# Kernel optimization log

Measured on AMD Instinct MI355X. Metric: run time of the kernel, lower is better.

Reference implementation:

```python
import jax, jax.numpy as jnp
import numpy as np


def setup_inputs() -> dict:
    key = jax.random.key(0)
    B, DP, N = 4, 3, 8192
    positions = jax.random.normal(key, (B, DP, N), dtype=jnp.float32)
    return {"positions": positions, "k": 16}


def reference(positions, k):
    # positions: [B, Dp, N] ('simple' data_format)
    # Pairwise squared Euclidean distances between all N points per batch:
    # d2[b, i, j] = ||x_i - x_j||^2 = ||x_i||^2 + ||x_j||^2 - 2 x_i . x_j
    sq = jnp.sum(positions * positions, axis=1)                     # [B, N]
    dots = jnp.einsum('bdn,bdm->bnm', positions, positions)         # [B, N, N]
    d2 = sq[:, :, None] + sq[:, None, :] - 2.0 * dots               # [B, N, N]
    # k nearest neighbors (smallest distance; includes self at distance ~0)
    neg_d, idx = jax.lax.top_k(-d2, k)                              # [B, N, K]
    # Layer transposes raw op output [B, N, K] -> [B, K, N]
    NN = jnp.transpose(idx, (0, 2, 1)).astype(jnp.int32)            # [B, K, N]
    distances = jnp.transpose(-neg_d, (0, 2, 1))                    # [B, K, N]
    return (NN, distances)
```

## Files before the change

kernel.cpp:

```cpp
#include <hip/hip_runtime.h>
#include <stdint.h>

#define NPTS 8192
#define NPAIR 4096
#define NB 4
#define KNN 16
#define RQ 2
#define CCAP 20
#define DCAP 256
#define MARGIN 1.5e-3f

typedef unsigned long long u64;
typedef unsigned int u32;
typedef unsigned short u16;
typedef float f32x2 __attribute__((ext_vector_type(2)));

__device__ __forceinline__ u32 f2ord(float f) {
    u32 b = __float_as_uint(f);
    return (b & 0x80000000u) ? ~b : (b | 0x80000000u);
}
__device__ __forceinline__ float ord2f(u32 u) {
    u32 b = (u & 0x80000000u) ? (u & 0x7fffffffu) : ~u;
    return __uint_as_float(b);
}
__device__ __forceinline__ u64 shflx64(u64 v, int m) {
    u32 lo = (u32)v, hi = (u32)(v >> 32);
    lo = __shfl_xor(lo, m, 64);
    hi = __shfl_xor(hi, m, 64);
    return ((u64)hi << 32) | lo;
}

__global__ __launch_bounds__(256) void pack_kernel(const float* __restrict__ pos,
                                                   float4* __restrict__ pos8) {
    int t = blockIdx.x * 256 + threadIdx.x;
    int b = t >> 12;
    int m = t & (NPAIR - 1);
    const float* p = pos + (size_t)b * 3 * NPTS;
    float2 x = *(const float2*)&p[2 * m];
    float2 y = *(const float2*)&p[NPTS + 2 * m];
    float2 z = *(const float2*)&p[2 * NPTS + 2 * m];
    float s0 = __fadd_rn(__fadd_rn(__fmul_rn(x.x, x.x), __fmul_rn(y.x, y.x)), __fmul_rn(z.x, z.x));
    float s1 = __fadd_rn(__fadd_rn(__fmul_rn(x.y, x.y), __fmul_rn(y.y, y.y)), __fmul_rn(z.y, z.y));
    pos8[2 * t]     = make_float4(x.x, x.y, y.x, y.y);
    pos8[2 * t + 1] = make_float4(z.x, z.y, s0, s1);
}

#define RECOMP2(r, m, d0, d1)                                                           \
    { float4 _a = P8[2 * (m)], _c = P8[2 * (m) + 1];                                    \
      float _dot0 = __fmaf_rn(qzv[r].x, _c.x, __fmaf_rn(qyv[r].x, _a.z, __fmul_rn(qxv[r].x, _a.x))); \
      float _dot1 = __fmaf_rn(qzv[r].x, _c.y, __fmaf_rn(qyv[r].x, _a.w, __fmul_rn(qxv[r].x, _a.y))); \
      d0 = __fsub_rn(__fadd_rn(qw[r], _c.z), __fmul_rn(2.0f, _dot0));                   \
      d1 = __fsub_rn(__fadd_rn(qw[r], _c.w), __fmul_rn(2.0f, _dot1)); }

#define PROC(Av, Cv, mm)                                                                \
    {                                                                                   \
        f32x2 x01 = {(Av).x, (Av).y}, y01 = {(Av).z, (Av).w};                           \
        f32x2 z01 = {(Cv).x, (Cv).y}, sq01 = {(Cv).z, (Cv).w};                          \
        _Pragma("unroll")                                                               \
        for (int r = 0; r < RQ; ++r) {                                                  \
            f32x2 dot01 = __builtin_elementwise_fma(                                    \
                qzv[r], z01, __builtin_elementwise_fma(qyv[r], y01, qxv[r] * x01));     \
            f32x2 val01 = __builtin_elementwise_fma(n2v, dot01, sq01);                  \
            col[wv][r][c[r]][lane] = (u16)(mm);                                         \
            c[r] += (fminf(val01.x, val01.y) < Tm[r]) ? 1 : 0;                          \
        }                                                                               \
    }

__global__ __launch_bounds__(256) void knn_kernel(const float4* __restrict__ pos8,
                                                  float* __restrict__ out) {
    __shared__ u16 col[4][RQ][CCAP][64];
    __shared__ u16 dense[4][DCAP];
    const int lane = threadIdx.x & 63;
    const int wv = threadIdx.x >> 6;
    const int rowbase = blockIdx.x * (4 * RQ) + wv * RQ;
    const int b = rowbase >> 13;
    const int ib = rowbase & (NPTS - 1);
    const float4* __restrict__ P8 = pos8 + (size_t)b * NPAIR * 2;
    const u64 below = (1ull << lane) - 1ull;

    f32x2 qxv[RQ], qyv[RQ], qzv[RQ];
    float qw[RQ];
    {
        int m = ib >> 1;
        float4 a = P8[2 * m], cc = P8[2 * m + 1];
        qxv[0] = (f32x2){a.x, a.x};  qyv[0] = (f32x2){a.z, a.z};
        qzv[0] = (f32x2){cc.x, cc.x}; qw[0] = cc.z;
        qxv[1] = (f32x2){a.y, a.y};  qyv[1] = (f32x2){a.w, a.w};
        qzv[1] = (f32x2){cc.y, cc.y}; qw[1] = cc.w;
    }
    const f32x2 n2v = {-2.0f, -2.0f};

    float Tm[RQ];
    int c[RQ];

    auto rank16f = [&](float v) -> float {
#pragma unroll
        for (int k = 2; k <= 64; k <<= 1)
#pragma unroll
            for (int j = k >> 1; j >= 1; j >>= 1) {
                float o = __shfl_xor(v, j, 64);
                bool up = ((lane & k) == 0) == ((lane & j) == 0);
                v = (up ? (v < o) : (v > o)) ? v : o;
            }
        return __shfl(v, 15, 64);
    };

    auto tighten = [&](int r) {
        u32 mn = 0xFFFFFFFFu;
#pragma unroll
        for (int t = 0; t < CCAP; ++t) {
            if (t < c[r]) {
                u32 m = (u32)col[wv][r][t][lane];
                float d0, d1; RECOMP2(r, m, d0, d1);
                u32 om = f2ord(d0); u32 o1 = f2ord(d1);
                om = o1 < om ? o1 : om;
                mn = om < mn ? om : mn;
            }
        }
        u32 v = mn;
#pragma unroll
        for (int k = 2; k <= 64; k <<= 1)
#pragma unroll
            for (int j = k >> 1; j >= 1; j >>= 1) {
                u32 o = (u32)__shfl_xor((int)v, j, 64);
                bool up = ((lane & k) == 0) == ((lane & j) == 0);
                v = (up ? (v < o) : (v > o)) ? v : o;
            }
        u32 ordK = (u32)__shfl((int)v, 15, 64);
        int nc = 0;
#pragma unroll
        for (int t = 0; t < CCAP; ++t) {
            if (t < c[r]) {
                u32 m = (u32)col[wv][r][t][lane];
                float d0, d1; RECOMP2(r, m, d0, d1);
                u32 om = f2ord(d0); u32 o1 = f2ord(d1);
                om = o1 < om ? o1 : om;
                if (om <= ordK) { col[wv][r][nc][lane] = (u16)m; ++nc; }
            }
        }
        c[r] = nc;
#pragma unroll 1
        for (int it = 0; it < CCAP - 16; ++it) {
            if (c[r] > 16) {
                u64 mx = 0; int mt = 0;
#pragma unroll
                for (int t = 0; t < CCAP; ++t) {
                    if (t < c[r]) {
                        u32 m = (u32)col[wv][r][t][lane];
                        float d0, d1; RECOMP2(r, m, d0, d1);
                        u32 o0 = f2ord(d0), o1 = f2ord(d1);
                        u64 key = (o1 < o0)
                            ? (((u64)o1 << 13) | (2 * m + 1))
                            : (((u64)o0 << 13) | (2 * m));
                        if (key > mx) { mx = key; mt = t; }
                    }
                }
                col[wv][r][mt][lane] = col[wv][r][c[r] - 1][lane];
                c[r] -= 1;
            }
        }
        Tm[r] = fminf(Tm[r], (ord2f(ordK) - qw[r]) + MARGIN);
    };

    {
        float4 A[4], C[4];
#pragma unroll
        for (int s = 0; s < 4; ++s) {
            int m = s * 64 + lane;
            A[s] = P8[2 * m];
            C[s] = P8[2 * m + 1];
        }
#pragma unroll
        for (int r = 0; r < RQ; ++r) {
            f32x2 vv[4];
            float mn = __uint_as_float(0x7f800000u);
#pragma unroll
            for (int s = 0; s < 4; ++s) {
                f32x2 x01 = {A[s].x, A[s].y}, y01 = {A[s].z, A[s].w};
                f32x2 z01 = {C[s].x, C[s].y}, sq01 = {C[s].z, C[s].w};
                vv[s] = __builtin_elementwise_fma(
                    n2v, __builtin_elementwise_fma(qzv[r], z01,
                         __builtin_elementwise_fma(qyv[r], y01, qxv[r] * x01)), sq01);
                mn = fminf(mn, fminf(vv[s].x, vv[s].y));
            }
            float V16 = rank16f(mn);
            Tm[r] = V16 + 2.0f * MARGIN;
            c[r] = 0;
#pragma unroll
            for (int s = 0; s < 4; ++s) {
                int m = s * 64 + lane;
                col[wv][r][c[r]][lane] = (u16)m;
                c[r] += (fminf(vv[s].x, vv[s].y) < Tm[r]) ? 1 : 0;
            }
        }
    }

#pragma unroll 1
    for (int g = 1; g < 16; ++g) {
        if (__ballot(c[0] > 16)) tighten(0);
        if (__ballot(c[1] > 16)) tighten(1);
        int base = g * 256;
        float4 A[4], C[4];
#pragma unroll
        for (int s = 0; s < 4; ++s) {
            int m = base + s * 64 + lane;
            A[s] = P8[2 * m];
            C[s] = P8[2 * m + 1];
        }
        PROC(A[0], C[0], base + lane);
        PROC(A[1], C[1], base + 64 + lane);
        PROC(A[2], C[2], base + 128 + lane);
        PROC(A[3], C[3], base + 192 + lane);
    }

#pragma unroll
    for (int r = 0; r < RQ; ++r) {
        int sum = c[r];
#pragma unroll
        for (int s2 = 1; s2 < 64; s2 <<= 1) sum += __shfl_xor(sum, s2, 64);
        if (sum > 32) tighten(r);
        int nc = 0;
#pragma unroll 1
        for (int t = 0; t < CCAP; ++t) {
            bool valid = t < c[r];
            u64 bal = __ballot(valid);
            if (!bal) break;
            if (valid) dense[wv][nc + (int)__popcll(bal & below)] = col[wv][r][t][lane];
            nc += (int)__popcll(bal);
        }
        u64 myk = ~0ULL;
        if (nc <= 32) {
            bool valid = lane < 2 * nc;
            u32 m = valid ? (u32)dense[wv][lane >> 1] : 0u;
            float d0, d1; RECOMP2(r, m, d0, d1);
            float dd = (lane & 1) ? d1 : d0;
            u64 v = valid ? (((u64)f2ord(dd) << 13) | (2 * m + (lane & 1))) : ~0ULL;
#pragma unroll
            for (int k = 2; k <= 64; k <<= 1)
#pragma unroll
                for (int j = k >> 1; j >= 1; j >>= 1) {
                    u64 o = shflx64(v, j);
                    bool up = ((lane & k) == 0) == ((lane & j) == 0);
                    v = (up ? (v < o) : (v > o)) ? v : o;
                }
            myk = v;
        } else {
            u64 s8[8];
#pragma unroll
            for (int t = 0; t < 4; ++t) {
                int bi = t * 64 + lane;
                bool valid = bi < nc;
                u32 m = valid ? (u32)dense[wv][bi] : 0u;
                float d0, d1; RECOMP2(r, m, d0, d1);
                s8[2 * t]     = valid ? (((u64)f2ord(d0) << 13) | (2 * m))     : ~0ULL;
                s8[2 * t + 1] = valid ? (((u64)f2ord(d1) << 13) | (2 * m + 1)) : ~0ULL;
            }
#pragma unroll 1
            for (int rr = 0; rr < KNN; ++rr) {
                u64 lm = s8[0];
#pragma unroll
                for (int t = 1; t < 8; ++t) lm = s8[t] < lm ? s8[t] : lm;
                u64 mm = lm;
#pragma unroll
                for (int s2 = 1; s2 < 64; s2 <<= 1) { u64 o = shflx64(mm, s2); mm = o < mm ? o : mm; }
#pragma unroll
                for (int t = 0; t < 8; ++t) s8[t] = (s8[t] == mm) ? ~0ULL : s8[t];
                if (lane == rr) myk = mm;
            }
        }
        if (lane < KNN) {
            int iq = ib + r;
            size_t o1 = (size_t)(b * KNN + lane) * NPTS + iq;
            out[o1] = (float)(u32)(myk & (u64)(NPTS - 1));
            out[(size_t)NB * KNN * NPTS + o1] = ord2f((u32)(myk >> 13));
        }
    }
}

extern "C" void kernel_launch(void* const* d_in, const int* in_sizes, int n_in,
                              void* d_out, int out_size, void* d_ws, size_t ws_size,
                              hipStream_t stream) {
    const float* pos = (const float*)d_in[0];
    float* out = (float*)d_out;
    float4* pos8 = (float4*)d_ws;

    pack_kernel<<<dim3(NB * NPAIR / 256), dim3(256), 0, stream>>>(pos, pos8);
    knn_kernel<<<dim3(NB * NPTS / 8), dim3(256), 0, stream>>>(pos8, out);
}
```

Baseline: 164.0 us.

## Stage candidate point tiles in double-buffered shared memory with prefetch

Before, each wave loaded all 256 candidate points of a tile straight from global memory, so the four waves of a block fetched the same data four times. Now the block loads each tile once, one point per thread, into SoA shared-memory buffers. The next tile is prefetched into registers while the current one is processed, and a block-wide barrier runs after every tile. This cuts redundant global/L2 traffic and hides load latency, at the cost of 8KB of LDS, per-tile __syncthreads, and waves becoming coupled even though tighten() is called per wave.

Result: no change. 166.3 us (+1.4%).

```diff
diff --git a/kernel.cpp b/kernel.cpp
--- a/kernel.cpp
+++ b/kernel.cpp
@@ -52,26 +52,29 @@
       d0 = __fsub_rn(__fadd_rn(qw[r], _c.z), __fmul_rn(2.0f, _dot0));                   \
       d1 = __fsub_rn(__fadd_rn(qw[r], _c.w), __fmul_rn(2.0f, _dot1)); }
 
-#define PROC(Av, Cv, mm)                                                                \
+#define PROCL(cur, s, gbase)                                                            \
     {                                                                                   \
-        f32x2 x01 = {(Av).x, (Av).y}, y01 = {(Av).z, (Av).w};                           \
-        f32x2 z01 = {(Cv).x, (Cv).y}, sq01 = {(Cv).z, (Cv).w};                          \
+        int idx = (s) * 64 + lane;                                                      \
+        f32x2 x01 = sxA[cur][idx], y01 = syA[cur][idx];                                 \
+        f32x2 z01 = szA[cur][idx], sq01 = sqA[cur][idx];                                \
         _Pragma("unroll")                                                               \
         for (int r = 0; r < RQ; ++r) {                                                  \
             f32x2 dot01 = __builtin_elementwise_fma(                                    \
                 qzv[r], z01, __builtin_elementwise_fma(qyv[r], y01, qxv[r] * x01));     \
             f32x2 val01 = __builtin_elementwise_fma(n2v, dot01, sq01);                  \
-            col[wv][r][c[r]][lane] = (u16)(mm);                                         \
+            col[wv][r][c[r]][lane] = (u16)((gbase) + idx);                              \
             c[r] += (fminf(val01.x, val01.y) < Tm[r]) ? 1 : 0;                          \
         }                                                                               \
     }
 
 __global__ __launch_bounds__(256) void knn_kernel(const float4* __restrict__ pos8,
                                                   float* __restrict__ out) {
+    __shared__ f32x2 sxA[2][256], syA[2][256], szA[2][256], sqA[2][256];
     __shared__ u16 col[4][RQ][CCAP][64];
     __shared__ u16 dense[4][DCAP];
-    const int lane = threadIdx.x & 63;
-    const int wv = threadIdx.x >> 6;
+    const int tid = threadIdx.x;
+    const int lane = tid & 63;
+    const int wv = tid >> 6;
     const int rowbase = blockIdx.x * (4 * RQ) + wv * RQ;
     const int b = rowbase >> 13;
     const int ib = rowbase & (NPTS - 1);
@@ -195,22 +198,40 @@
         }
     }
 
+    {
+        int p = 256 + tid;
+        float4 a = P8[2 * p], cc = P8[2 * p + 1];
+        sxA[1][tid] = (f32x2){a.x, a.y};
+        syA[1][tid] = (f32x2){a.z, a.w};
+        szA[1][tid] = (f32x2){cc.x, cc.y};
+        sqA[1][tid] = (f32x2){cc.z, cc.w};
+    }
+    __syncthreads();
+
 #pragma unroll 1
     for (int g = 1; g < 16; ++g) {
+        int cur = g & 1;
+        float4 na, nc2;
+        if (g < 15) {
+            int p = (g + 1) * 256 + tid;
+            na = P8[2 * p];
+            nc2 = P8[2 * p + 1];
+        }
         if (__ballot(c[0] > 16)) tighten(0);
         if (__ballot(c[1] > 16)) tighten(1);
-        int base = g * 256;
-        float4 A[4], C[4];
-#pragma unroll
-        for (int s = 0; s < 4; ++s) {
-            int m = base + s * 64 + lane;
-            A[s] = P8[2 * m];
-            C[s] = P8[2 * m + 1];
-        }
-        PROC(A[0], C[0], base + lane);
-        PROC(A[1], C[1], base + 64 + lane);
-        PROC(A[2], C[2], base + 128 + lane);
-        PROC(A[3], C[3], base + 192 + lane);
+        int gbase = g * 256;
+        PROCL(cur, 0, gbase);
+        PROCL(cur, 1, gbase);
+        PROCL(cur, 2, gbase);
+        PROCL(cur, 3, gbase);
+        if (g < 15) {
+            int nxt = cur ^ 1;
+            sxA[nxt][tid] = (f32x2){na.x, na.y};
+            syA[nxt][tid] = (f32x2){na.z, na.w};
+            szA[nxt][tid] = (f32x2){nc2.x, nc2.y};
+            sqA[nxt][tid] = (f32x2){nc2.z, nc2.w};
+        }
+        __syncthreads();
     }
 
 #pragma unroll
```
